# Kernel optimization log

Hardware: AMD Instinct MI355X
Metric: run time of the kernel (lower is better)

## Reference

```python
import jax, jax.numpy as jnp
import numpy as np

B, S, E, NH = 2, 2048, 1024, 16
THETA = 10000.0


def setup_inputs() -> dict:
    key = jax.random.key(0)
    k1, k2 = jax.random.split(key, 2)
    hidden_states = jax.random.normal(k1, (B, S, E), dtype=jnp.float32)
    in_proj_weight = jax.random.normal(k2, (3 * E, E), dtype=jnp.float32) * 0.02
    in_proj_bias = jnp.zeros((3 * E,), dtype=jnp.float32)
    return {
        "hidden_states": hidden_states,
        "in_proj_weight": in_proj_weight,
        "in_proj_bias": in_proj_bias,
        "T": 1,
        "H": 32,
        "W": 64,
    }


def _rope(x, cos, sin):
    # x: [BT, seq, n_heads, head_dim]; cos/sin: [seq, head_dim//2]
    # pairs are consecutive elements (x[2i], x[2i+1]) == complex (re, im)
    xr = x.reshape(x.shape[:-1] + (-1, 2))
    xe, xo = xr[..., 0], xr[..., 1]
    c = cos[None, :, None, :]
    s = sin[None, :, None, :]
    re = xe * c - xo * s
    im = xe * s + xo * c
    return jnp.stack([re, im], axis=-1).reshape(x.shape)


def reference(hidden_states, in_proj_weight, in_proj_bias, T, H, W):
    Bx, Sx, Ex = hidden_states.shape
    hd = Ex // NH
    # fused QKV projection
    qkv = hidden_states @ in_proj_weight.T + in_proj_bias
    q, k, v = jnp.split(qkv, 3, axis=-1)
    # 1D rotary over chunks of length S//T (T=1 -> full sequence)
    seq = Sx // T
    inv_freq = 1.0 / (THETA ** (jnp.arange(0, hd, 2, dtype=jnp.float32) / hd))
    ang = jnp.arange(seq, dtype=jnp.float32)[:, None] * inv_freq  # [seq, hd//2]
    cos, sin = jnp.cos(ang), jnp.sin(ang)
    q = _rope(q.reshape(Bx * T, seq, NH, hd), cos, sin).reshape(Bx, Sx, NH, hd)
    k = _rope(k.reshape(Bx * T, seq, NH, hd), cos, sin).reshape(Bx, Sx, NH, hd)
    v = v.reshape(Bx, Sx, NH, hd)
    # scaled dot-product attention (special_attn encoder path: no out_proj)
    scale = 1.0 / jnp.sqrt(jnp.asarray(hd, dtype=jnp.float32))
    scores = jnp.einsum('bqnd,bknd->bnqk', q, k) * scale
    attn = jax.nn.softmax(scores, axis=-1)
    out = jnp.einsum('bnqk,bknd->bqnd', attn, v)
    return out.reshape(Bx, Sx, Ex)
```

## Files before the change

### kernel.cpp

```cpp
#include <hip/hip_runtime.h>
#include <math.h>

#define BB 2
#define SS 2048
#define EE 1024
#define NHH 16
#define HD 64
#define HD2 32

typedef _Float16 f16x8 __attribute__((ext_vector_type(8)));
typedef __attribute__((ext_vector_type(4))) float f32x4;

static __device__ __forceinline__ unsigned pkh(float a, float b) {
    union { _Float16 h[2]; unsigned u; } v;
    v.h[0] = (_Float16)a; v.h[1] = (_Float16)b;
    return v.u;
}

static __device__ __forceinline__ void dma16(const void* g, void* l) {
    __builtin_amdgcn_global_load_lds(
        (const __attribute__((address_space(1))) unsigned int*)g,
        (__attribute__((address_space(3))) unsigned int*)l,
        16, 0, 0);
}

__global__ __launch_bounds__(256) void rope_table_k(float* __restrict__ ct,
                                                    float* __restrict__ st) {
    int idx = blockIdx.x * 256 + threadIdx.x;
    if (idx >= SS * HD2) return;
    int s = idx >> 5, p = idx & 31;
    double inv = pow(10000.0, -(double)(2 * p) / 64.0);
    double ang = (double)s * inv;
    ct[idx] = (float)cos(ang);
    st[idx] = (float)sin(ang);
}

__global__ __launch_bounds__(256, 3) void qkv_mfma_k(
    const float* __restrict__ X, const float* __restrict__ W,
    const float* __restrict__ bias,
    const float* __restrict__ ct, const float* __restrict__ st,
    unsigned short* __restrict__ Qg, unsigned short* __restrict__ Kg,
    unsigned short* __restrict__ Vg)
{
    __shared__ __align__(16) unsigned short Alds[4096];
    __shared__ __align__(16) unsigned short Blds[4096];

    const int tid  = threadIdx.x;
    const int wave = tid >> 6;
    const int lane = tid & 63;
    const int quad = lane >> 4;
    const int l15  = lane & 15;
    const int m0   = blockIdx.y * 128;
    const int n0b  = blockIdx.x * 128;

    const int r  = tid >> 1;
    const int ks = (tid & 1) * 16;
    const int q0s = ks >> 3;
    const int grp_s = r >> 4;
    const int l15s  = r & 15;

    const float* ap = X + (size_t)(m0 + r) * EE + ks;
    const float* bp = W + (size_t)(n0b + r) * EE + ks;

    f32x4 acc[4][4];
#pragma unroll
    for (int mc = 0; mc < 4; mc++)
#pragma unroll
        for (int nc = 0; nc < 4; nc++) acc[mc][nc] = (f32x4){0.f, 0.f, 0.f, 0.f};

    float4 a[4], bb[4];
#pragma unroll
    for (int i = 0; i < 4; i++) {
        a[i]  = *(const float4*)(ap + i * 4);
        bb[i] = *(const float4*)(bp + i * 4);
    }

    const int mg = (wave >> 1) * 4;
    const int ng = (wave & 1) * 4;

    for (int kt = 0; kt < EE / 32; kt++) {
        __syncthreads();
#pragma unroll
        for (int half = 0; half < 2; half++) {
            int q = q0s + half;
            const float* fa = (const float*)&a[half * 2];
            const float* fb = (const float*)&bb[half * 2];
            unsigned uaw[4], ubw[4];
#pragma unroll
            for (int jj = 0; jj < 4; jj++) {
                uaw[jj] = pkh(fa[2 * jj], fa[2 * jj + 1]);
                ubw[jj] = pkh(fb[2 * jj], fb[2 * jj + 1]);
            }
            int e = (grp_s * 4 + q) * 128 + l15s * 8;
            *(uint4*)(Alds + e) = make_uint4(uaw[0], uaw[1], uaw[2], uaw[3]);
            *(uint4*)(Blds + e) = make_uint4(ubw[0], ubw[1], ubw[2], ubw[3]);
        }
        __syncthreads();

        if (kt < EE / 32 - 1) {
            ap += 32; bp += 32;
#pragma unroll
            for (int i = 0; i < 4; i++) {
                a[i]  = *(const float4*)(ap + i * 4);
                bb[i] = *(const float4*)(bp + i * 4);
            }
        }

        f16x8 Af[4], Bf[4];
#pragma unroll
        for (int mc = 0; mc < 4; mc++)
            Af[mc] = *(const f16x8*)(Alds + ((mg + mc) * 4 + quad) * 128 + l15 * 8);
#pragma unroll
        for (int nc = 0; nc < 4; nc++)
            Bf[nc] = *(const f16x8*)(Blds + ((ng + nc) * 4 + quad) * 128 + l15 * 8);
#pragma unroll
        for (int mc = 0; mc < 4; mc++)
#pragma unroll
            for (int nc = 0; nc < 4; nc++)
                acc[mc][nc] = __builtin_amdgcn_mfma_f32_16x16x32_f16(Af[mc], Bf[nc], acc[mc][nc], 0, 0, 0);
    }

    const int n0w = n0b + (wave & 1) * 64;
    const int m0w = m0 + (wave >> 1) * 64;
    const int sec = n0w >> 10;
    const int h   = (n0w & 1023) >> 6;
    const int bq  = m0w >> 11;
    const size_t abase = (size_t)(bq * NHH + h) * 131072;
    unsigned short* dst = (sec == 0) ? Qg : (sec == 1) ? Kg : Vg;

    float bn[4];
#pragma unroll
    for (int nc = 0; nc < 4; nc++) bn[nc] = bias[n0w + nc * 16 + l15];

    if (sec < 2) {
        const float scq = (sec == 0) ? 0.18033688f : 1.0f;
#pragma unroll
        for (int mc = 0; mc < 4; mc++) {
            int sb = (m0w & 2047) + mc * 16;
#pragma unroll
            for (int nc = 0; nc < 4; nc++) {
                int d = nc * 16 + l15;
                int p = d >> 1;
                int kc_d = d >> 5, quad_a = (d >> 3) & 3, j = d & 7;
#pragma unroll
                for (int rr = 0; rr < 4; rr++) {
                    int srow = sb + quad * 4 + rr;
                    float x = acc[mc][nc][rr] + bn[nc];
                    float xp = __shfl_xor(x, 1);
                    float c = ct[srow * 32 + p], sn = st[srow * 32 + p];
                    float o = ((l15 & 1) == 0) ? (x * c - xp * sn) : (xp * sn + x * c);
                    o *= scq;
                    float op = __shfl_xor(o, 1);
                    if ((l15 & 1) == 0) {
                        unsigned u = pkh(o, op);
                        size_t e = abase +
                            (size_t)((((srow >> 4) * 2 + kc_d) * 4 + quad_a)) * 128 +
                            (srow & 15) * 8 + j;
                        *(unsigned int*)(dst + e) = u;
                    }
                }
            }
        }
    } else {
#pragma unroll
        for (int mc = 0; mc < 4; mc++) {
            int sb = (m0w & 2047) + mc * 16;
            int s32 = sb >> 5;
            int quad_v = ((sb >> 3) + (quad >> 1)) & 3;
            int j0 = (quad & 1) * 4;
#pragma unroll
            for (int nc = 0; nc < 4; nc++) {
                float x0 = acc[mc][nc][0] + bn[nc];
                float x1 = acc[mc][nc][1] + bn[nc];
                float x2 = acc[mc][nc][2] + bn[nc];
                float x3 = acc[mc][nc][3] + bn[nc];
                unsigned u01 = pkh(x0, x1), u23 = pkh(x2, x3);
                size_t e = abase +
                    (size_t)(((s32 * 4 + nc) * 4 + quad_v)) * 128 + l15 * 8 + j0;
                *(uint2*)(dst + e) = make_uint2(u01, u23);
            }
        }
    }
}

__global__ __launch_bounds__(128, 2) void attn_mfma_k(
    const unsigned short* __restrict__ Qg,
    const unsigned short* __restrict__ Kg,
    const unsigned short* __restrict__ Vg,
    float* __restrict__ out)
{
    __shared__ __align__(16) unsigned short Klds[4096];
    __shared__ __align__(16) unsigned short Pbuf[2][1088];

    const int tid  = threadIdx.x;
    const int wave = tid >> 6;
    const int lane = tid & 63;
    const int quad = lane >> 4;
    const int l15  = lane & 15;
    const int id   = blockIdx.x;
    const int bh   = (id & 7) * 4 + ((id >> 3) & 3);
    const int qt   = id >> 5;
    const int b    = bh >> 4, h = bh & 15;
    const int q_wave = qt * 64 + wave * 32;
    const size_t abase = (size_t)bh * 131072;

    f16x8 qf[2][2];
#pragma unroll
    for (int nc = 0; nc < 2; nc++)
#pragma unroll
        for (int kc = 0; kc < 2; kc++)
            qf[nc][kc] = *(const f16x8*)(Qg + abase +
                (size_t)(((((q_wave >> 4) + nc) * 2 + kc) * 4 + quad)) * 128 + l15 * 8);

    f32x4 acc[2][4];
#pragma unroll
    for (int nc = 0; nc < 2; nc++)
#pragma unroll
        for (int dc = 0; dc < 4; dc++) acc[nc][dc] = (f32x4){0.f, 0.f, 0.f, 0.f};
    float mst[2] = {-INFINITY, -INFINITY};
    float lst[2] = {0.f, 0.f};

    const unsigned short* kgb = Kg + abase;
    const unsigned short* vgb = Vg + abase;

    for (int kt = 0; kt < SS / 64; kt++) {
        __syncthreads();
#pragma unroll
        for (int i = 0; i < 4; i++)
            dma16(kgb + (size_t)kt * 4096 + (tid + i * 128) * 8,
                  Klds + (tid + i * 128) * 8);
        __syncthreads();

        const unsigned short* vt = vgb + (size_t)kt * 4096;
        f16x8 vf[4][2];
#pragma unroll
        for (int dc = 0; dc < 4; dc++)
#pragma unroll
            for (int kk2 = 0; kk2 < 2; kk2++)
                vf[dc][kk2] = *(const f16x8*)(vt + (kk2 * 16 + dc * 4 + quad) * 128 + l15 * 8);

        f32x4 stt[2][4];
#pragma unroll
        for (int mc = 0; mc < 4; mc++) {
            f16x8 a0 = *(const f16x8*)(Klds + ((mc * 2 + 0) * 4 + quad) * 128 + l15 * 8);
            f16x8 a1 = *(const f16x8*)(Klds + ((mc * 2 + 1) * 4 + quad) * 128 + l15 * 8);
#pragma unroll
            for (int nc = 0; nc < 2; nc++) {
                f32x4 s = (f32x4){0.f, 0.f, 0.f, 0.f};
                s = __builtin_amdgcn_mfma_f32_16x16x32_f16(a0, qf[nc][0], s, 0, 0, 0);
                s = __builtin_amdgcn_mfma_f32_16x16x32_f16(a1, qf[nc][1], s, 0, 0, 0);
                stt[nc][mc] = s;
            }
        }

#pragma unroll
        for (int nc = 0; nc < 2; nc++) {
            float mt = -INFINITY;
#pragma unroll
            for (int mc = 0; mc < 4; mc++)
#pragma unroll
                for (int rr = 0; rr < 4; rr++) mt = fmaxf(mt, stt[nc][mc][rr]);
            mt = fmaxf(mt, __shfl_xor(mt, 16));
            mt = fmaxf(mt, __shfl_xor(mt, 32));
            float mnew = fmaxf(mst[nc], mt);
            float alpha = __builtin_amdgcn_exp2f(mst[nc] - mnew);
            float p[4][4];
            float ps = 0.f;
#pragma unroll
            for (int mc = 0; mc < 4; mc++)
#pragma unroll
                for (int rr = 0; rr < 4; rr++) {
                    float e = __builtin_amdgcn_exp2f(stt[nc][mc][rr] - mnew);
                    p[mc][rr] = e;
                    ps += e;
                }
            ps += __shfl_xor(ps, 16);
            ps += __shfl_xor(ps, 32);
            lst[nc] = lst[nc] * alpha + ps;
            mst[nc] = mnew;

            float ar[4];
#pragma unroll
            for (int rr = 0; rr < 4; rr++)
                ar[rr] = __shfl(alpha, (lane & 48) + ((lane >> 4) << 2) + rr);
#pragma unroll
            for (int dc = 0; dc < 4; dc++)
#pragma unroll
                for (int rr = 0; rr < 4; rr++) acc[nc][dc][rr] *= ar[rr];

            unsigned short* Pw = Pbuf[wave];
#pragma unroll
            for (int mc = 0; mc < 4; mc++)
#pragma unroll
                for (int pr = 0; pr < 2; pr++) {
                    unsigned u = pkh(p[mc][2 * pr], p[mc][2 * pr + 1]);
                    int kk2 = mc >> 1;
                    int quadp = (mc & 1) * 2 + (quad >> 1);
                    int j = (quad & 1) * 4 + 2 * pr;
                    *(unsigned int*)(Pw + (kk2 * 4 + quadp) * 136 + l15 * 8 + j) = u;
                }
            f16x8 pf[2];
#pragma unroll
            for (int kk2 = 0; kk2 < 2; kk2++)
                pf[kk2] = *(const f16x8*)(Pw + (kk2 * 4 + quad) * 136 + l15 * 8);

#pragma unroll
            for (int dc = 0; dc < 4; dc++) {
                f32x4 aa = acc[nc][dc];
#pragma unroll
                for (int kk2 = 0; kk2 < 2; kk2++)
                    aa = __builtin_amdgcn_mfma_f32_16x16x32_f16(pf[kk2], vf[dc][kk2], aa, 0, 0, 0);
                acc[nc][dc] = aa;
            }
        }
    }

#pragma unroll
    for (int nc = 0; nc < 2; nc++) {
        float linv = 1.f / lst[nc];
        float lr[4];
#pragma unroll
        for (int rr = 0; rr < 4; rr++)
            lr[rr] = __shfl(linv, (lane & 48) + ((lane >> 4) << 2) + rr);
#pragma unroll
        for (int dc = 0; dc < 4; dc++)
#pragma unroll
            for (int rr = 0; rr < 4; rr++) {
                int s = q_wave + nc * 16 + quad * 4 + rr;
                out[((size_t)(b * SS + s)) * EE + h * HD + dc * 16 + l15] = acc[nc][dc][rr] * lr[rr];
            }
    }
}

extern "C" void kernel_launch(void* const* d_in, const int* in_sizes, int n_in,
                              void* d_out, int out_size, void* d_ws, size_t ws_size,
                              hipStream_t stream) {
    const float* X    = (const float*)d_in[0];
    const float* W    = (const float*)d_in[1];
    const float* bias = (const float*)d_in[2];
    float* out = (float*)d_out;

    float* ws = (float*)d_ws;
    float* ct = ws;
    float* st = ws + 65536;
    unsigned short* base = (unsigned short*)(ws + 131072);
    const size_t ASZ = (size_t)32 * 131072;
    unsigned short* Qg = base;
    unsigned short* Kg = base + ASZ;
    unsigned short* Vg = base + 2 * ASZ;

    rope_table_k<<<(SS * HD2 + 255) / 256, 256, 0, stream>>>(ct, st);
    qkv_mfma_k<<<dim3(3 * EE / 128, BB * SS / 128), 256, 0, stream>>>(
        X, W, bias, ct, st, Qg, Kg, Vg);
    attn_mfma_k<<<dim3(1024), 128, 0, stream>>>(Qg, Kg, Vg, out);
}
```

Baseline: 215.9 us.

## Pre-convert X and W to tiled fp16 and DMA tiles directly into LDS

Adds a separate conversion kernel that casts X and W to fp16 and lays them out in the exact tiled order used by the GEMM's shared-memory tiles. The QKV GEMM then loads each tile with global_load_lds DMA instead of loading fp32, converting in registers and storing to LDS. The launch also becomes a 1D grid remapped so tiles sharing N are grouped per XCD, aiming for better L2 reuse. In exchange it costs an extra kernel launch plus a full read and write of X and W, and it drops the register prefetch, so global loads are no longer overlapped with MFMA work.

```diff
diff --git a/kernel.cpp b/kernel.cpp
--- a/kernel.cpp
+++ b/kernel.cpp
@@ -35,8 +35,31 @@
     st[idx] = (float)sin(ang);
 }
 
+#define NXCHUNK 524288
+#define NWCHUNK 393216
+__global__ __launch_bounds__(256) void cvt_k(
+    const float* __restrict__ X, const float* __restrict__ W,
+    unsigned short* __restrict__ Xh, unsigned short* __restrict__ Wh)
+{
+    int idx = blockIdx.x * 256 + threadIdx.x;
+    const float* src;
+    unsigned short* dst;
+    int c;
+    if (idx < NXCHUNK) { src = X; dst = Xh; c = idx; }
+    else               { src = W; dst = Wh; c = idx - NXCHUNK;
+                         if (c >= NWCHUNK) return; }
+    int l15 = c & 15, q = (c >> 4) & 3, grp = (c >> 6) & 7;
+    int kt = (c >> 9) & 31, t = c >> 14;
+    int row = t * 128 + grp * 16 + l15;
+    int k   = kt * 32 + q * 8;
+    float4 v0 = *(const float4*)(src + (size_t)row * EE + k);
+    float4 v1 = *(const float4*)(src + (size_t)row * EE + k + 4);
+    *(uint4*)(dst + (size_t)c * 8) =
+        make_uint4(pkh(v0.x, v0.y), pkh(v0.z, v0.w), pkh(v1.x, v1.y), pkh(v1.z, v1.w));
+}
+
 __global__ __launch_bounds__(256, 3) void qkv_mfma_k(
-    const float* __restrict__ X, const float* __restrict__ W,
+    const unsigned short* __restrict__ Xh, const unsigned short* __restrict__ Wh,
     const float* __restrict__ bias,
     const float* __restrict__ ct, const float* __restrict__ st,
     unsigned short* __restrict__ Qg, unsigned short* __restrict__ Kg,
@@ -50,61 +73,35 @@
     const int lane = tid & 63;
     const int quad = lane >> 4;
     const int l15  = lane & 15;
-    const int m0   = blockIdx.y * 128;
-    const int n0b  = blockIdx.x * 128;
-
-    const int r  = tid >> 1;
-    const int ks = (tid & 1) * 16;
-    const int q0s = ks >> 3;
-    const int grp_s = r >> 4;
-    const int l15s  = r & 15;
-
-    const float* ap = X + (size_t)(m0 + r) * EE + ks;
-    const float* bp = W + (size_t)(n0b + r) * EE + ks;
+
+    const int id    = blockIdx.x;
+    const int xcd   = id & 7;
+    const int local = id >> 3;
+    const int nt    = xcd * 3 + local % 3;
+    const int mt    = local / 3;
+    const int m0    = mt * 128;
+    const int n0b   = nt * 128;
 
     f32x4 acc[4][4];
 #pragma unroll
     for (int mc = 0; mc < 4; mc++)
 #pragma unroll
         for (int nc = 0; nc < 4; nc++) acc[mc][nc] = (f32x4){0.f, 0.f, 0.f, 0.f};
-
-    float4 a[4], bb[4];
-#pragma unroll
-    for (int i = 0; i < 4; i++) {
-        a[i]  = *(const float4*)(ap + i * 4);
-        bb[i] = *(const float4*)(bp + i * 4);
-    }
 
     const int mg = (wave >> 1) * 4;
     const int ng = (wave & 1) * 4;
 
     for (int kt = 0; kt < EE / 32; kt++) {
         __syncthreads();
-#pragma unroll
-        for (int half = 0; half < 2; half++) {
-            int q = q0s + half;
-            const float* fa = (const float*)&a[half * 2];
-            const float* fb = (const float*)&bb[half * 2];
-            unsigned uaw[4], ubw[4];
-#pragma unroll
-            for (int jj = 0; jj < 4; jj++) {
-                uaw[jj] = pkh(fa[2 * jj], fa[2 * jj + 1]);
-                ubw[jj] = pkh(fb[2 * jj], fb[2 * jj + 1]);
-            }
-            int e = (grp_s * 4 + q) * 128 + l15s * 8;
-            *(uint4*)(Alds + e) = make_uint4(uaw[0], uaw[1], uaw[2], uaw[3]);
-            *(uint4*)(Blds + e) = make_uint4(ubw[0], ubw[1], ubw[2], ubw[3]);
+        {
+            const unsigned short* at = Xh + ((size_t)(mt * 32 + kt)) * 4096;
+            const unsigned short* bt = Wh + ((size_t)(nt * 32 + kt)) * 4096;
+            dma16(at + (size_t)tid * 8,         Alds + tid * 8);
+            dma16(at + (size_t)(tid + 256) * 8, Alds + (tid + 256) * 8);
+            dma16(bt + (size_t)tid * 8,         Blds + tid * 8);
+            dma16(bt + (size_t)(tid + 256) * 8, Blds + (tid + 256) * 8);
         }
         __syncthreads();
-
-        if (kt < EE / 32 - 1) {
-            ap += 32; bp += 32;
-#pragma unroll
-            for (int i = 0; i < 4; i++) {
-                a[i]  = *(const float4*)(ap + i * 4);
-                bb[i] = *(const float4*)(bp + i * 4);
-            }
-        }
 
         f16x8 Af[4], Bf[4];
 #pragma unroll
@@ -348,9 +345,12 @@
     unsigned short* Qg = base;
     unsigned short* Kg = base + ASZ;
     unsigned short* Vg = base + 2 * ASZ;
+    unsigned short* Xh = base + 3 * ASZ;
+    unsigned short* Wh = Xh + (size_t)NXCHUNK * 8;
 
     rope_table_k<<<(SS * HD2 + 255) / 256, 256, 0, stream>>>(ct, st);
-    qkv_mfma_k<<<dim3(3 * EE / 128, BB * SS / 128), 256, 0, stream>>>(
-        X, W, bias, ct, st, Qg, Kg, Vg);
+    cvt_k<<<(NXCHUNK + NWCHUNK) / 256, 256, 0, stream>>>(X, W, Xh, Wh);
+    qkv_mfma_k<<<dim3(768), 256, 0, stream>>>(
+        Xh, Wh, bias, ct, st, Qg, Kg, Vg);
     attn_mfma_k<<<dim3(1024), 128, 0, stream>>>(Qg, Kg, Vg, out);
 }
```

New measurement: 188.6 us. 1.14x faster.
